# Kernel optimization log

Hardware: AMD Instinct MI355X
Metric: run time of the kernel (lower is better)

The kernel has to match this reference:

```python
import jax, jax.numpy as jnp
import numpy as np

STRIDE = 1
PAD = 1
DIL = 1


def setup_inputs() -> dict:
    key = jax.random.key(0)
    k1, k2, k3, k4, k5 = jax.random.split(key, 5)
    B, Cin, D, H, W = 1, 32, 16, 56, 56
    Cout, K = 64, 27  # 3x3x3 kernel
    x = jax.random.normal(k1, (B, Cin, D, H, W), jnp.float32)
    # offset-predicting conv: 3*offset_groups*K output channels (dz,dy,dx per kernel pt)
    # (module inits these to zero; we use small random values to exercise interpolation)
    offset_w = jax.random.normal(k2, (3 * K, Cin, 3, 3, 3), jnp.float32) * 0.02
    offset_b = jax.random.normal(k3, (3 * K,), jnp.float32) * 0.02
    weight = jax.random.normal(k4, (Cout, Cin, 3, 3, 3), jnp.float32) / np.sqrt(Cin * K).astype(np.float32)
    bias = jax.random.normal(k5, (Cout,), jnp.float32) * 0.01
    return {"x": x, "offset_w": offset_w, "offset_b": offset_b, "weight": weight, "bias": bias}


def _trilinear_sample(xc, coords):
    # xc: [C, D, H, W]; coords: [K, P, 3] float (z, y, x) in input voxel space.
    # Zero padding outside bounds (torchvision deform_conv convention).
    C, D, H, W = xc.shape
    xf = xc.reshape(C, D * H * W)
    z, y, x = coords[..., 0], coords[..., 1], coords[..., 2]
    z0, y0, x0 = jnp.floor(z), jnp.floor(y), jnp.floor(x)
    fz, fy, fx = z - z0, y - y0, x - x0
    acc = jnp.zeros((C,) + z.shape, xc.dtype)
    for dz in (0, 1):
        wz = fz if dz else 1.0 - fz
        zi = z0 + dz
        for dy in (0, 1):
            wy = fy if dy else 1.0 - fy
            yi = y0 + dy
            for dx in (0, 1):
                wx = fx if dx else 1.0 - fx
                xi = x0 + dx
                valid = (zi >= 0) & (zi < D) & (yi >= 0) & (yi < H) & (xi >= 0) & (xi < W)
                idx = ((jnp.clip(zi, 0, D - 1) * H + jnp.clip(yi, 0, H - 1)) * W
                       + jnp.clip(xi, 0, W - 1)).astype(jnp.int32)
                w = (wz * wy * wx) * valid.astype(xc.dtype)
                acc = acc + w[None] * xf[:, idx]  # gather -> [C, K, P]
    return acc


def _forward(x, offset_w, offset_b, weight, bias):
    B, Cin, D, H, W = x.shape
    Cout = weight.shape[0]
    kd, kh, kw = weight.shape[2:]
    K = kd * kh * kw
    # dense Conv3d predicting offsets: [B, 3K, Do, Ho, Wo]
    off = jax.lax.conv_general_dilated(
        x, offset_w, (STRIDE,) * 3, [(PAD, PAD)] * 3, rhs_dilation=(DIL,) * 3,
        dimension_numbers=("NCDHW", "OIDHW", "NCDHW")) + offset_b[None, :, None, None, None]
    Do, Ho, Wo = off.shape[2:]
    P = Do * Ho * Wo
    off = off.reshape(B, K, 3, P).transpose(0, 1, 3, 2)  # [B, K, P, 3] (dz,dy,dx)
    # base sampling grid per kernel point
    kz, ky, kx = jnp.meshgrid(jnp.arange(kd), jnp.arange(kh), jnp.arange(kw), indexing="ij")
    kz, ky, kx = kz.reshape(K), ky.reshape(K), kx.reshape(K)
    gz, gy, gx = jnp.meshgrid(jnp.arange(Do) * STRIDE - PAD,
                              jnp.arange(Ho) * STRIDE - PAD,
                              jnp.arange(Wo) * STRIDE - PAD, indexing="ij")
    pz = (kz * DIL)[:, None] + gz.reshape(-1)[None]  # [K, P]
    py = (ky * DIL)[:, None] + gy.reshape(-1)[None]
    px = (kx * DIL)[:, None] + gx.reshape(-1)[None]
    base = jnp.stack([pz, py, px], axis=-1).astype(off.dtype)  # [K, P, 3]
    coords = off + base[None]  # [B, K, P, 3]
    sampled = jax.vmap(_trilinear_sample)(x, coords)  # [B, Cin, K, P]
    out = jnp.einsum("bckp,ock->bop", sampled, weight.reshape(Cout, Cin, K)) + bias[None, :, None]
    return out.reshape(B, Cout, Do, Ho, Wo)


def reference(x, offset_w, offset_b, weight, bias):
    return _forward(x, offset_w, offset_b, weight, bias)
```

## Files before the change

kernel.cpp:

```cpp
#include <hip/hip_runtime.h>
#include <math.h>

#define D_   16
#define H_   56
#define W_   56
#define CIN  32
#define COUT 64
#define KPTS 27
#define NCH  81
#define NP   (D_*H_*W_)
#define CHW  (D_*H_*W_)
#define KPAD 28

typedef float f4 __attribute__((ext_vector_type(4)));

static __device__ __forceinline__ int iclamp(int v, int lo, int hi) {
    return v < lo ? lo : (v > hi ? hi : v);
}

__global__ __launch_bounds__(256) void k_prep(const float* __restrict__ w,
                                              const float* __restrict__ ow,
                                              float* __restrict__ wT,
                                              float* __restrict__ owT) {
    int i = blockIdx.x * 256 + threadIdx.x;
    if (i < COUT * CIN * KPTS) {
        int tap = i % KPTS;
        int c   = (i / KPTS) % CIN;
        int o   = i / (KPTS * CIN);
        wT[(tap * CIN + c) * COUT + o] = w[i];
    }
    if (i < NCH * CIN * KPTS) {
        int tap = i % KPTS;
        int c   = (i / KPTS) % CIN;
        int ch  = i / (KPTS * CIN);
        int d   = ch % 3;
        int kpt = ch / 3;
        owT[(((tap * 3) + d) * CIN + c) * KPAD + kpt] = ow[i];
    }
    if (i < KPTS * 3 * CIN)
        owT[i * KPAD + 27] = 0.0f;
}

__global__ __launch_bounds__(256) void k_init(const float* __restrict__ bias,
                                              float* __restrict__ out) {
    const int i   = blockIdx.x * 256 + threadIdx.x;
    const float b = bias[(i * 4) / NP];
    f4 v; v.x = b; v.y = b; v.z = b; v.w = b;
    ((f4*)out)[i] = v;
}

__global__ __launch_bounds__(64, 2) void k_offsets(const float* __restrict__ x,
                                                   const float* __restrict__ owT,
                                                   const float* __restrict__ offb,
                                                   float* __restrict__ coords) {
    const int tid = threadIdx.x;
    const int p   = blockIdx.x * 64 + tid;
    const int d   = blockIdx.y;
    const int ox  = p % W_;
    const int t   = p / W_;
    const int oy  = t % H_;
    const int oz  = t / H_;

    f4 A0, A1, A2, A3, A4, A5, A6;
#define INIT4(Ai, kb) { f4 v; \
    v.x = offb[((kb) + 0) * 3 + d]; \
    v.y = offb[((kb) + 1) * 3 + d]; \
    v.z = offb[((kb) + 2) * 3 + d]; \
    v.w = ((kb) + 3 < KPTS) ? offb[((kb) + 3) * 3 + d] : 0.0f; \
    Ai = v; }
    INIT4(A0, 0) INIT4(A1, 4) INIT4(A2, 8) INIT4(A3, 12)
    INIT4(A4, 16) INIT4(A5, 20) INIT4(A6, 24)
#undef INIT4

    for (int tap = 0; tap < KPTS; ++tap) {
        const int kz = tap / 9, ky = (tap / 3) % 3, kx = tap % 3;
        const int zi = oz - 1 + kz, yi = oy - 1 + ky, xi = ox - 1 + kx;
        const bool val = ((unsigned)zi < (unsigned)D_) &&
                         ((unsigned)yi < (unsigned)H_) &&
                         ((unsigned)xi < (unsigned)W_);
        const int sidx = (iclamp(zi, 0, D_ - 1) * H_ + iclamp(yi, 0, H_ - 1)) * W_
                       + iclamp(xi, 0, W_ - 1);
        const float m = val ? 1.0f : 0.0f;

        const f4* w4 = (const f4*)(owT + (size_t)((tap * 3 + d) * CIN) * KPAD);
#pragma unroll 4
        for (int c = 0; c < CIN; ++c) {
            const float xv = m * x[c * CHW + sidx];
            const f4* wp = w4 + c * 7;
            A0 += wp[0] * xv; A1 += wp[1] * xv; A2 += wp[2] * xv;
            A3 += wp[3] * xv; A4 += wp[4] * xv; A5 += wp[5] * xv;
            A6 += wp[6] * xv;
        }
    }

#define BASEF(kk) ((d == 0) ? (float)(oz - 1 + (kk) / 9) \
                 : (d == 1) ? (float)(oy - 1 + ((kk) / 3) % 3) \
                            : (float)(ox - 1 + (kk) % 3))
#define WOUT(Ai, kb) { \
    coords[(d * KPTS + (kb) + 0) * NP + p] = Ai.x + BASEF((kb) + 0); \
    coords[(d * KPTS + (kb) + 1) * NP + p] = Ai.y + BASEF((kb) + 1); \
    coords[(d * KPTS + (kb) + 2) * NP + p] = Ai.z + BASEF((kb) + 2); \
    if ((kb) + 3 < KPTS) \
        coords[(d * KPTS + (kb) + 3) * NP + p] = Ai.w + BASEF((kb) + 3); }
    WOUT(A0, 0) WOUT(A1, 4) WOUT(A2, 8) WOUT(A3, 12)
    WOUT(A4, 16) WOUT(A5, 20) WOUT(A6, 24)
#undef WOUT
#undef BASEF
}

__global__ __launch_bounds__(64, 2) void k_dconv(const float* __restrict__ x,
                                                 const float* __restrict__ coords,
                                                 const float* __restrict__ wT,
                                                 float* __restrict__ out) {
    const int tid = threadIdx.x;
    const int p   = blockIdx.x * 64 + tid;
    const int g   = blockIdx.y;

    f4 A0 = 0, A1 = 0, A2 = 0, A3 = 0, A4 = 0, A5 = 0, A6 = 0, A7 = 0;
    f4 A8 = 0, A9 = 0, A10 = 0, A11 = 0, A12 = 0, A13 = 0, A14 = 0, A15 = 0;

    for (int tap = 9 * g; tap < 9 * g + 9; ++tap) {
        const float cz = coords[(0 * KPTS + tap) * NP + p];
        const float cy = coords[(1 * KPTS + tap) * NP + p];
        const float cx = coords[(2 * KPTS + tap) * NP + p];

        const float zf = floorf(cz), yf = floorf(cy), xf = floorf(cx);
        const float fz = cz - zf, fy = cy - yf, fx = cx - xf;
        const int z0 = (int)zf, y0 = (int)yf, x0 = (int)xf;

        float cw0, cw1, cw2, cw3, cw4, cw5, cw6, cw7;
        int   cb0, cb1, cb2, cb3, cb4, cb5, cb6, cb7;
#define CORNER(jj, Wj, Bj) { \
    const int dz_ = (jj) >> 2, dy_ = ((jj) >> 1) & 1, dx_ = (jj) & 1; \
    const int zi_ = z0 + dz_, yi_ = y0 + dy_, xi_ = x0 + dx_; \
    const bool v_ = ((unsigned)zi_ < (unsigned)D_) && \
                    ((unsigned)yi_ < (unsigned)H_) && \
                    ((unsigned)xi_ < (unsigned)W_); \
    const float wz_ = dz_ ? fz : 1.0f - fz; \
    const float wy_ = dy_ ? fy : 1.0f - fy; \
    const float wx_ = dx_ ? fx : 1.0f - fx; \
    Wj = v_ ? wz_ * wy_ * wx_ : 0.0f; \
    Bj = (iclamp(zi_, 0, D_ - 1) * H_ + iclamp(yi_, 0, H_ - 1)) * W_ \
         + iclamp(xi_, 0, W_ - 1); }
        CORNER(0, cw0, cb0) CORNER(1, cw1, cb1) CORNER(2, cw2, cb2)
        CORNER(3, cw3, cb3) CORNER(4, cw4, cb4) CORNER(5, cw5, cb5)
        CORNER(6, cw6, cb6) CORNER(7, cw7, cb7)
#undef CORNER

        const float* wtap = wT + (size_t)tap * CIN * COUT;
#pragma unroll 4
        for (int c = 0; c < CIN; ++c) {
            const float* xc = x + c * CHW;
            const float v0 = xc[cb0], v1 = xc[cb1], v2 = xc[cb2], v3 = xc[cb3];
            const float v4 = xc[cb4], v5 = xc[cb5], v6 = xc[cb6], v7 = xc[cb7];
            const float s = cw0 * v0 + cw1 * v1 + cw2 * v2 + cw3 * v3
                          + cw4 * v4 + cw5 * v5 + cw6 * v6 + cw7 * v7;
            const f4* wq = (const f4*)(wtap + c * COUT);
            A0  += wq[0]  * s; A1  += wq[1]  * s; A2  += wq[2]  * s; A3  += wq[3]  * s;
            A4  += wq[4]  * s; A5  += wq[5]  * s; A6  += wq[6]  * s; A7  += wq[7]  * s;
            A8  += wq[8]  * s; A9  += wq[9]  * s; A10 += wq[10] * s; A11 += wq[11] * s;
            A12 += wq[12] * s; A13 += wq[13] * s; A14 += wq[14] * s; A15 += wq[15] * s;
        }
    }

    float* op = out + p;
#define AOUT(Ai, ob) { \
    atomicAdd(op + ((ob) + 0) * NP, Ai.x); atomicAdd(op + ((ob) + 1) * NP, Ai.y); \
    atomicAdd(op + ((ob) + 2) * NP, Ai.z); atomicAdd(op + ((ob) + 3) * NP, Ai.w); }
    AOUT(A0, 0)  AOUT(A1, 4)  AOUT(A2, 8)   AOUT(A3, 12)
    AOUT(A4, 16) AOUT(A5, 20) AOUT(A6, 24)  AOUT(A7, 28)
    AOUT(A8, 32) AOUT(A9, 36) AOUT(A10, 40) AOUT(A11, 44)
    AOUT(A12, 48) AOUT(A13, 52) AOUT(A14, 56) AOUT(A15, 60)
#undef AOUT
}

extern "C" void kernel_launch(void* const* d_in, const int* in_sizes, int n_in,
                              void* d_out, int out_size, void* d_ws, size_t ws_size,
                              hipStream_t stream) {
    const float* x    = (const float*)d_in[0];
    const float* offw = (const float*)d_in[1];
    const float* offb = (const float*)d_in[2];
    const float* wgt  = (const float*)d_in[3];
    const float* bias = (const float*)d_in[4];
    float* out = (float*)d_out;

    float* ws     = (float*)d_ws;
    float* coords = ws;
    float* wT     = coords + 3 * KPTS * NP;
    float* owT    = wT + KPTS * CIN * COUT;

    const int n_tr = NCH * CIN * KPTS;
    hipLaunchKernelGGL(k_prep, dim3((n_tr + 255) / 256), dim3(256), 0, stream,
                       wgt, offw, wT, owT);
    hipLaunchKernelGGL(k_init, dim3(COUT * NP / 4 / 256), dim3(256), 0, stream,
                       bias, out);
    hipLaunchKernelGGL(k_offsets, dim3(NP / 64, 3), dim3(64), 0, stream,
                       x, owT, offb, coords);
    hipLaunchKernelGGL(k_dconv, dim3(NP / 64, 3), dim3(64), 0, stream,
                       x, coords, wT, out);
}
```

Before: 583.9 us.

## Split offset and deform-conv tap loops across more blocks with atomic accumulation

The offset conv now splits its 27 taps into three groups of 9 across extra grid rows. Partial sums are atomically added into coords, which a new init kernel pre-fills with bias plus base grid. The deform conv splits taps into nine groups of 3 instead of three groups of 9. This raises block count and parallelism on the GPU, at the cost of more atomics to coords and out, one extra kernel launch, and repeated per-block setup.

```diff
diff --git a/kernel.cpp b/kernel.cpp
--- a/kernel.cpp
+++ b/kernel.cpp
@@ -49,30 +49,39 @@
     ((f4*)out)[i] = v;
 }
 
+__global__ __launch_bounds__(256) void k_init_coords(const float* __restrict__ offb,
+                                                     float* __restrict__ coords) {
+    const int i  = blockIdx.x * 256 + threadIdx.x;
+    const int p  = i % NP;
+    const int ck = i / NP;
+    const int d  = ck / KPTS;
+    const int k  = ck % KPTS;
+    const int kz = k / 9, ky = (k / 3) % 3, kx = k % 3;
+    const int x  = p % W_;
+    const int y  = (p / W_) % H_;
+    const int z  = p / (W_ * H_);
+    const float base = (d == 0) ? (float)(z - 1 + kz)
+                     : (d == 1) ? (float)(y - 1 + ky)
+                                : (float)(x - 1 + kx);
+    coords[i] = offb[k * 3 + d] + base;
+}
+
 __global__ __launch_bounds__(64, 2) void k_offsets(const float* __restrict__ x,
                                                    const float* __restrict__ owT,
-                                                   const float* __restrict__ offb,
                                                    float* __restrict__ coords) {
     const int tid = threadIdx.x;
     const int p   = blockIdx.x * 64 + tid;
-    const int d   = blockIdx.y;
+    const int by  = blockIdx.y;
+    const int d   = by / 3;
+    const int tg  = by % 3;
     const int ox  = p % W_;
     const int t   = p / W_;
     const int oy  = t % H_;
     const int oz  = t / H_;
 
-    f4 A0, A1, A2, A3, A4, A5, A6;
-#define INIT4(Ai, kb) { f4 v; \
-    v.x = offb[((kb) + 0) * 3 + d]; \
-    v.y = offb[((kb) + 1) * 3 + d]; \
-    v.z = offb[((kb) + 2) * 3 + d]; \
-    v.w = ((kb) + 3 < KPTS) ? offb[((kb) + 3) * 3 + d] : 0.0f; \
-    Ai = v; }
-    INIT4(A0, 0) INIT4(A1, 4) INIT4(A2, 8) INIT4(A3, 12)
-    INIT4(A4, 16) INIT4(A5, 20) INIT4(A6, 24)
-#undef INIT4
-
-    for (int tap = 0; tap < KPTS; ++tap) {
+    f4 A0 = 0, A1 = 0, A2 = 0, A3 = 0, A4 = 0, A5 = 0, A6 = 0;
+
+    for (int tap = 9 * tg; tap < 9 * tg + 9; ++tap) {
         const int kz = tap / 9, ky = (tap / 3) % 3, kx = tap % 3;
         const int zi = oz - 1 + kz, yi = oy - 1 + ky, xi = ox - 1 + kx;
         const bool val = ((unsigned)zi < (unsigned)D_) &&
@@ -93,19 +102,15 @@
         }
     }
 
-#define BASEF(kk) ((d == 0) ? (float)(oz - 1 + (kk) / 9) \
-                 : (d == 1) ? (float)(oy - 1 + ((kk) / 3) % 3) \
-                            : (float)(ox - 1 + (kk) % 3))
-#define WOUT(Ai, kb) { \
-    coords[(d * KPTS + (kb) + 0) * NP + p] = Ai.x + BASEF((kb) + 0); \
-    coords[(d * KPTS + (kb) + 1) * NP + p] = Ai.y + BASEF((kb) + 1); \
-    coords[(d * KPTS + (kb) + 2) * NP + p] = Ai.z + BASEF((kb) + 2); \
-    if ((kb) + 3 < KPTS) \
-        coords[(d * KPTS + (kb) + 3) * NP + p] = Ai.w + BASEF((kb) + 3); }
-    WOUT(A0, 0) WOUT(A1, 4) WOUT(A2, 8) WOUT(A3, 12)
-    WOUT(A4, 16) WOUT(A5, 20) WOUT(A6, 24)
-#undef WOUT
-#undef BASEF
+    float* cp = coords + (size_t)d * KPTS * NP + p;
+#define COUTA(Ai, kb) { \
+    atomicAdd(cp + ((kb) + 0) * NP, Ai.x); \
+    atomicAdd(cp + ((kb) + 1) * NP, Ai.y); \
+    atomicAdd(cp + ((kb) + 2) * NP, Ai.z); \
+    if ((kb) + 3 < KPTS) atomicAdd(cp + ((kb) + 3) * NP, Ai.w); }
+    COUTA(A0, 0) COUTA(A1, 4) COUTA(A2, 8) COUTA(A3, 12)
+    COUTA(A4, 16) COUTA(A5, 20) COUTA(A6, 24)
+#undef COUTA
 }
 
 __global__ __launch_bounds__(64, 2) void k_dconv(const float* __restrict__ x,
@@ -119,7 +124,7 @@
     f4 A0 = 0, A1 = 0, A2 = 0, A3 = 0, A4 = 0, A5 = 0, A6 = 0, A7 = 0;
     f4 A8 = 0, A9 = 0, A10 = 0, A11 = 0, A12 = 0, A13 = 0, A14 = 0, A15 = 0;
 
-    for (int tap = 9 * g; tap < 9 * g + 9; ++tap) {
+    for (int tap = 3 * g; tap < 3 * g + 3; ++tap) {
         const float cz = coords[(0 * KPTS + tap) * NP + p];
         const float cy = coords[(1 * KPTS + tap) * NP + p];
         const float cx = coords[(2 * KPTS + tap) * NP + p];
@@ -194,8 +199,10 @@
                        wgt, offw, wT, owT);
     hipLaunchKernelGGL(k_init, dim3(COUT * NP / 4 / 256), dim3(256), 0, stream,
                        bias, out);
-    hipLaunchKernelGGL(k_offsets, dim3(NP / 64, 3), dim3(64), 0, stream,
-                       x, owT, offb, coords);
-    hipLaunchKernelGGL(k_dconv, dim3(NP / 64, 3), dim3(64), 0, stream,
+    hipLaunchKernelGGL(k_init_coords, dim3(NCH * NP / 256), dim3(256), 0, stream,
+                       offb, coords);
+    hipLaunchKernelGGL(k_offsets, dim3(NP / 64, 9), dim3(64), 0, stream,
+                       x, owT, coords);
+    hipLaunchKernelGGL(k_dconv, dim3(NP / 64, 9), dim3(64), 0, stream,
                        x, coords, wT, out);
 }
```

After: 537.2 us. 1.09x faster.
